# Kernel tuning notes

Measured on AMD Instinct MI355X. Metric: run time of the kernel, lower is better.

The kernel has to match this reference:

```python
import jax, jax.numpy as jnp
import numpy as np

EPS_ATTN = 1e-8  # self.eps is undefined in the torch source; standard slot-attention value
LN_EPS = 1e-5


def _ln(x, g=None, b=None, axes=(-1,)):
    m = x.mean(axes, keepdims=True)
    v = ((x - m) ** 2).mean(axes, keepdims=True)
    y = (x - m) * jax.lax.rsqrt(v + LN_EPS)
    return y * g + b if g is not None else y


def setup_inputs() -> dict:
    key = jax.random.key(0)
    ks = jax.random.split(key, 16)
    B, N, S, d, dh = 16, 4096, 8, 64, 128

    def w(k, shape, fan_in):
        return jax.random.normal(k, shape, jnp.float32) / np.float32(np.sqrt(fan_in))

    return {
        "inputs": jax.random.normal(ks[0], (B, N, d + 2), jnp.float32),
        "slots": jax.random.normal(ks[1], (S, d + 4), jnp.float32),
        "Wq": w(ks[2], (d, d), d),
        "Wk": w(ks[3], (d, d), d),
        "Wv": w(ks[4], (d, d), d),
        "Wg": w(ks[5], (d, 2), 2),
        "bg": jnp.zeros((d,), jnp.float32),
        "ln_pos_g": jnp.ones((d,), jnp.float32),
        "ln_pos_b": jnp.zeros((d,), jnp.float32),
        "W1": w(ks[6], (dh, d), d),
        "b1": jnp.zeros((dh,), jnp.float32),
        "W2": w(ks[7], (d, dh), dh),
        "b2": jnp.zeros((d,), jnp.float32),
        "W_ih": w(ks[8], (3 * d, d), d),
        "W_hh": w(ks[9], (3 * d, d), d),
        "b_ih": jnp.zeros((3 * d,), jnp.float32),
        "b_hh": jnp.zeros((3 * d,), jnp.float32),
        "ln_mlp_g": jnp.ones((d,), jnp.float32),
        "ln_mlp_b": jnp.zeros((d,), jnp.float32),
        "W3": w(ks[10], (dh, d), d),
        "b3": jnp.zeros((dh,), jnp.float32),
        "W4": w(ks[11], (d, dh), dh),
        "b4": jnp.zeros((d,), jnp.float32),
        "ln_slot_g": jnp.ones((d,), jnp.float32),
        "ln_slot_b": jnp.zeros((d,), jnp.float32),
        "n_iters": 3,
    }


def reference(inputs, slots, Wq, Wk, Wv, Wg, bg, ln_pos_g, ln_pos_b, W1, b1, W2, b2,
              W_ih, W_hh, b_ih, b_hh, ln_mlp_g, ln_mlp_b, W3, b3, W4, b4,
              ln_slot_g, ln_slot_b, n_iters):
    feats, grids = inputs[..., :-2], inputs[..., -2:]          # (B,N,d), (B,N,2)
    sl, pos, sc = slots[..., :-4], slots[..., -4:-2], slots[..., -2:]
    B, N, _ = feats.shape
    S, d = sl.shape
    scale = d ** (-0.5)

    slots = jnp.broadcast_to(sl, (B, S, d))
    positions = jnp.clip(jnp.broadcast_to(pos, (B, S, 2)), -1.0, 1.0)
    scales = jnp.clip(jnp.broadcast_to(sc, (B, S, 2)), 1e-3, 2.0)

    k = feats @ Wk.T                                           # (B,N,d)
    v = feats @ Wv.T

    def pos_mlp(x):  # LayerNorm -> Linear -> ReLU -> Linear
        h = _ln(x, ln_pos_g, ln_pos_b)
        h = jax.nn.relu(h @ W1.T + b1)
        return h @ W2.T + b2

    for i_iter in range(n_iters + 1):
        rel = (grids[:, :, None] - positions[:, None]) / scales[:, None]  # (B,N,S,2)
        rgp = rel @ Wg.T + bg                                             # (B,N,S,d)
        k_pos = pos_mlp(k[:, :, None] + rgp)                              # (B,N,S,d)
        v_pos = pos_mlp(v[:, :, None] + rgp)

        slots_n = _ln(slots, ln_slot_g, ln_slot_b)
        q = _ln(slots_n, axes=(-2, -1)) @ Wq.T                            # (B,S,d)

        dots = jnp.einsum('bsd,bnsd->bns', q, k_pos) * scale              # (B,N,S)
        attn = jax.nn.softmax(dots, axis=1) + EPS_ATTN
        attn = attn / attn.sum(axis=-1, keepdims=True)

        updates = jnp.einsum('bns,bnsd->bsd', attn, v_pos)                # (B,S,d)
        positions = jnp.einsum('bns,bnp->bsp', attn, grids)               # (B,S,2)
        spread = (grids[:, :, None] - positions[:, None]) ** 2            # (B,N,S,2)
        scales = jnp.clip(jnp.sqrt(jnp.einsum('bns,bnsp->bsp', attn, spread)), 1e-3, 2.0)

        if i_iter < n_iters:
            x = updates.reshape(-1, d)
            h = slots.reshape(-1, d)
            gi = x @ W_ih.T + b_ih
            gh = h @ W_hh.T + b_hh
            i_r, i_z, i_n = jnp.split(gi, 3, axis=-1)
            h_r, h_z, h_n = jnp.split(gh, 3, axis=-1)
            r = jax.nn.sigmoid(i_r + h_r)
            z = jax.nn.sigmoid(i_z + h_z)
            n_g = jnp.tanh(i_n + r * h_n)
            slots = ((1.0 - z) * n_g + z * h).reshape(B, S, d)
            # slot_mlp (no residual in the source)
            hmlp = jax.nn.relu(_ln(slots, ln_mlp_g, ln_mlp_b) @ W3.T + b3)
            slots = hmlp @ W4.T + b4

    return jnp.concatenate([slots, positions, scales], axis=-1)           # (B,S,d+4)
```

## Files before the change

kernel.cpp:

```cpp
#include <hip/hip_runtime.h>
#include <math.h>

#define BB 16
#define NN 4096
#define SS 8
#define DD 64
#define DHH 128
#define CIN 66
#define NITERS 3
#define LN_EPS_F 1e-5f
#define EPS_ATTN_F 1e-8f
#define QSCALE 0.125f
#define LO_SCALE 2048.0f
#define LO_INV 4.8828125e-4f

typedef __attribute__((ext_vector_type(8))) _Float16 half8;
typedef __attribute__((ext_vector_type(4))) float f32x4;
union H8 { half8 v; _Float16 u[8]; };

__device__ __forceinline__ float dot4(float4 a, float4 b) {
    return fmaf(a.x, b.x, fmaf(a.y, b.y, fmaf(a.z, b.z, a.w * b.w)));
}

__device__ __forceinline__ void split_fp16(float z, _Float16& h, _Float16& l) {
// ... 1 lines not shown
    float rem = (z - (float)hh) * LO_SCALE;
    h = hh;
    l = (_Float16)rem;
}

__global__ __launch_bounds__(256) void k_init_slots(
    const float* __restrict__ slots_in, float* __restrict__ slots,
    float* __restrict__ positions, float* __restrict__ scales) {
    int tid = blockIdx.x * 256 + threadIdx.x;
    if (tid < BB * SS * DD) {
        int s = (tid / DD) % SS;
        int c = tid % DD;
        slots[tid] = slots_in[s * 68 + c];
    }
    if (tid < BB * SS * 2) {
        int s = (tid >> 1) & 7;
        int p = tid & 1;
        float po = slots_in[s * 68 + 64 + p];
        positions[tid] = fminf(fmaxf(po, -1.f), 1.f);
        float sc = slots_in[s * 68 + 66 + p];
        scales[tid] = fminf(fmaxf(sc, 1e-3f), 2.f);
    }
}

__global__ __launch_bounds__(256) void k_prep_w(
    const float* __restrict__ W1, const float* __restrict__ lpg,
    const float* __restrict__ lpb, const float* __restrict__ b1,
    const float* __restrict__ Wg,
    float* __restrict__ W1p, float* __restrict__ avec, float* __restrict__ bvec,
    float* __restrict__ s1vec, float* __restrict__ b1p, float* __restrict__ wgc) {
    __shared__ float w1s[128 * 68];
    int tid = threadIdx.x;
    for (int q = 0; q < 8; q++) {
        int flat = q * 1024 + tid * 4;
        int o = flat >> 6, c = flat & 63;
        *(float4*)(w1s + o * 68 + c) = *(const float4*)(W1 + flat);
    }
    __syncthreads();
    if (tid < 128) {
        int o = tid;
        float a = 0.f, bv = 0.f, s1 = 0.f, b1a = b1[o];
        for (int c = 0; c < 64; c++) {
            float w0 = w1s[o * 68 + c];
            float w = w0 * lpg[c];
            W1p[o * 64 + c] = w;
            a = fmaf(w, Wg[2 * c], a);
            bv = fmaf(w, Wg[2 * c + 1], bv);
            s1 += w;
            b1a = fmaf(w0, lpb[c], b1a);
        }
        avec[o] = a; bvec[o] = bv; s1vec[o] = s1; b1p[o] = b1a;
    }
    if (tid == 128) {
        float mwA = 0.f, mwB = 0.f, AA = 0.f, BBv = 0.f, AB = 0.f;
        for (int c = 0; c < 64; c++) {
            float wa = Wg[2 * c], wb = Wg[2 * c + 1];
            mwA += wa; mwB += wb;
            AA = fmaf(wa, wa, AA); BBv = fmaf(wb, wb, BBv); AB = fmaf(wa, wb, AB);
        }
        wgc[0] = mwA * (1.f / 64.f);
        wgc[1] = mwB * (1.f / 64.f);
        wgc[2] = AA * (1.f / 64.f);
        wgc[3] = BBv * (1.f / 64.f);
        wgc[4] = AB * (2.f / 64.f);
    }
}

__global__ __launch_bounds__(256) void k_prep_w2(
    const float* __restrict__ W1p, const float* __restrict__ Wk,
    const float* __restrict__ Wv, const float* __restrict__ bg,
    float* __restrict__ Wall, float* __restrict__ cu) {
    int flat = blockIdx.x * 256 + threadIdx.x;
    int mat = flat >> 13, rem = flat & 8191;
    int o = rem >> 6, c = rem & 63;
    const float* Wm = mat ? Wv : Wk;
    float acc = 0.f;
    for (int d = 0; d < 64; d++)
        acc = fmaf(W1p[o * 64 + d], Wm[d * 64 + c], acc);
    Wall[flat] = acc;
    if (flat < 128) {
        float a = 0.f;
        for (int d = 0; d < 64; d++) a = fmaf(W1p[flat * 64 + d], bg[d], a);
        cu[flat] = a;
    }
}

__global__ __launch_bounds__(256) void k_prep_frag(
    const float* __restrict__ Wall, const float* __restrict__ Wk,
    const float* __restrict__ Wv,
    _Float16* __restrict__ cwh, _Float16* __restrict__ cwl,
    _Float16* __restrict__ mwh, _Float16* __restrict__ mwl) {
    int idx = blockIdx.x * 256 + threadIdx.x;
    if (idx < 2048) {
        int f = idx >> 6, lane = idx & 63;
        int m = f >> 4, rest = f & 15;
        int ot = rest >> 1, ks = rest & 1;
        int o = ot * 16 + (lane & 15);
        int k0 = ks * 32 + (lane >> 4) * 8;
        const float* src = Wall + m * 8192 + o * 64 + k0;
        #pragma unroll
        for (int j = 0; j < 8; j++) {
            _Float16 h, l;
            split_fp16(src[j], h, l);
            cwh[(size_t)f * 512 + lane * 8 + j] = h;
            cwl[(size_t)f * 512 + lane * 8 + j] = l;
        }
    } else if (idx < 3072) {
        int id2 = idx - 2048;
        int f = id2 >> 6, lane = id2 & 63;
        int m = f >> 3, rest = f & 7;
        int ot = rest >> 1, ks = rest & 1;
        int o = ot * 16 + (lane & 15);
        int k0 = ks * 32 + (lane >> 4) * 8;
        const float* src = (m ? Wv : Wk) + o * 64 + k0;
        #pragma unroll
        for (int j = 0; j < 8; j++) {
            _Float16 h, l;
            split_fp16(src[j], h, l);
            mwh[(size_t)f * 512 + lane * 8 + j] = h;
            mwl[(size_t)f * 512 + lane * 8 + j] = l;
        }
    }
}

__global__ __launch_bounds__(256) void k_prep_mfma(
    const float* __restrict__ inp,
    const _Float16* __restrict__ cwh, const _Float16* __restrict__ cwl,
    const _Float16* __restrict__ mwh, const _Float16* __restrict__ mwl,
    const float* __restrict__ cu, const float* __restrict__ bg,
    const float* __restrict__ Wg,
    float* __restrict__ uk, float* __restrict__ uv,
    float* __restrict__ kaux, float* __restrict__ vaux, float* __restrict__ gbuf) {
    int tid = threadIdx.x;
    int wv = tid >> 6, lane = tid & 63;
    int quad = lane >> 4, col = lane & 15;
    int mat = blockIdx.y;
    int rowTile = blockIdx.x * 64 + wv * 16;
    half8 ah[2], al[2];
    {
        int rA = rowTile + col;
        const float* rp = inp + (size_t)rA * CIN + quad * 8;
        #pragma unroll
        for (int ks = 0; ks < 2; ks++) {
            H8 h, l;
            #pragma unroll
            for (int q = 0; q < 4; q++) {
                float2 v = *(const float2*)(rp + ks * 32 + 2 * q);
                split_fp16(v.x, h.u[2 * q], l.u[2 * q]);
                split_fp16(v.y, h.u[2 * q + 1], l.u[2 * q + 1]);
            }
            ah[ks] = h.v; al[ks] = l.v;
        }
    }
    const _Float16* cwhm = cwh + (size_t)mat * 16 * 512;
    const _Float16* cwlm = cwl + (size_t)mat * 16 * 512;
    float* dst = mat ? uv : uk;
    float* outb = dst + (size_t)(rowTile + quad * 4) * 128 + col;
    #pragma unroll
    for (int ot = 0; ot < 8; ot++) {
        f32x4 acc1 = {0.f, 0.f, 0.f, 0.f}, acc2 = {0.f, 0.f, 0.f, 0.f};
        #pragma unroll
        for (int ks = 0; ks < 2; ks++) {
            half8 bh = *(const half8*)(cwhm + (size_t)(ot * 2 + ks) * 512 + lane * 8);
            half8 bl = *(const half8*)(cwlm + (size_t)(ot * 2 + ks) * 512 + lane * 8);
            acc1 = __builtin_amdgcn_mfma_f32_16x16x32_f16(ah[ks], bh, acc1, 0, 0, 0);
            acc2 = __builtin_amdgcn_mfma_f32_16x16x32_f16(al[ks], bh, acc2, 0, 0, 0);
// ... 100 lines not shown
    w2q[(b * SS + s) * DHH + c] = a0 * QSCALE;
    w2q[(b * SS + s) * DHH + c + 64] = a1 * QSCALE;
    float qb = qv[s][c] * b2[c];
    for (int off = 32; off; off >>= 1) qb += __shfl_xor(qb, off, 64);
    if (c == 0) qb2[b * SS + s] = qb * QSCALE;
}

__global__ __launch_bounds__(256) void k_pass1(
    const float* __restrict__ uk, const float* __restrict__ kaux,
    const float* __restrict__ positions, const float* __restrict__ scales,
    const float* __restrict__ avec, const float* __restrict__ bvec,
    const float* __restrict__ s1vec, const float* __restrict__ b1p,
    const float* __restrict__ wgc, const float* __restrict__ w2q,
    const float* __restrict__ qb2, float* __restrict__ dots) {
    int tid = threadIdx.x;
    int chunk = blockIdx.x, b = blockIdx.y;
    int wv = tid >> 6, lane = tid & 63, rh = lane >> 5, ol = lane & 31;
    int o4 = ol * 4;
    float4 a4 = *(const float4*)(avec + o4);
    float4 bv4 = *(const float4*)(bvec + o4);
    float4 s14 = *(const float4*)(s1vec + o4);
    float4 b14 = *(const float4*)(b1p + o4);
    float mwA = wgc[0], mwB = wgc[1], AA = wgc[2], BBc = wgc[3], AB2 = wgc[4];
    float p0[8], p1[8], rc0[8], rc1[8], qb[8];
    float4 wq[8];
    #pragma unroll
    for (int s = 0; s < 8; s++) {
        int bs = b * 8 + s;
        p0[s] = positions[bs * 2]; p1[s] = positions[bs * 2 + 1];
        rc0[s] = 1.f / scales[bs * 2]; rc1[s] = 1.f / scales[bs * 2 + 1];
        qb[s] = qb2[bs];
        wq[s] = *(const float4*)(w2q + (size_t)bs * DHH + o4);
    }
    int row0 = chunk * 64 + wv * 16 + rh;
    size_t rg = (size_t)b * NN + row0;
    float4 m1 = *(const float4*)(kaux + rg * 8);
    float4 m2 = *(const float4*)(kaux + rg * 8 + 4);
    float4 u4 = *(const float4*)(uk + rg * 128 + o4);
    for (int st = 0; st < 8; st++) {
        float4 n1, n2, nu;
        if (st < 7) {
            size_t rgn = rg + (size_t)(st + 1) * 2;
            n1 = *(const float4*)(kaux + rgn * 8);
            n2 = *(const float4*)(kaux + rgn * 8 + 4);
            nu = *(const float4*)(uk + rgn * 128 + o4);
        }
        int row = row0 + st * 2;
        #pragma unroll
        for (int s = 0; s < 8; s++) {
            float rel0 = (m2.x - p0[s]) * rc0[s];
            float rel1 = (m2.y - p1[s]) * rc1[s];
            float m = fmaf(rel1, mwB, fmaf(rel0, mwA, m1.x));
            float q2 = fmaf(rel0, fmaf(rel0, AA, m1.z), m1.y);
            q2 = fmaf(rel1, fmaf(rel1, BBc, m1.w), q2);
            q2 = fmaf(rel0 * rel1, AB2, q2);
            float var = fmaf(-m, m, q2);
            float rstd = rsqrtf(fmaxf(var, 0.f) + LN_EPS_F);
            float p = 0.f, t, h;
            t = fmaf(-m, s14.x, u4.x); t = fmaf(rel0, a4.x, t); t = fmaf(rel1, bv4.x, t);
            h = fmaf(rstd, t, b14.x); p = fmaf(fmaxf(h, 0.f), wq[s].x, p);
            t = fmaf(-m, s14.y, u4.y); t = fmaf(rel0, a4.y, t); t = fmaf(rel1, bv4.y, t);
            h = fmaf(rstd, t, b14.y); p = fmaf(fmaxf(h, 0.f), wq[s].y, p);
            t = fmaf(-m, s14.z, u4.z); t = fmaf(rel0, a4.z, t); t = fmaf(rel1, bv4.z, t);
            h = fmaf(rstd, t, b14.z); p = fmaf(fmaxf(h, 0.f), wq[s].z, p);
            t = fmaf(-m, s14.w, u4.w); t = fmaf(rel0, a4.w, t); t = fmaf(rel1, bv4.w, t);
            h = fmaf(rstd, t, b14.w); p = fmaf(fmaxf(h, 0.f), wq[s].w, p);
            p += __shfl_xor(p, 1, 64);
            p += __shfl_xor(p, 2, 64);
            p += __shfl_xor(p, 4, 64);
            p += __shfl_xor(p, 8, 64);
            p += __shfl_xor(p, 16, 64);
            if (ol == 0)
                dots[(size_t)(b * 8 + s) * NN + row] = p + qb[s];
        }
        m1 = n1; m2 = n2; u4 = nu;
    }
}

__global__ __launch_bounds__(256) void k_pass2(
    const float* __restrict__ uv, const float* __restrict__ vaux,
    const float* __restrict__ positions, const float* __restrict__ scales,
    const float* __restrict__ avec, const float* __restrict__ bvec,
    const float* __restrict__ s1vec, const float* __restrict__ b1p,
    const float* __restrict__ wgc, const float* __restrict__ attn,
    float* __restrict__ H) {
    __shared__ float Hw[4 * 1024];
    int tid = threadIdx.x;
    int chunk = blockIdx.x, b = blockIdx.y;
    int wv = tid >> 6, lane = tid & 63, rh = lane >> 5, ol = lane & 31;
    int o4 = ol * 4;
    float4 a4 = *(const float4*)(avec + o4);
    float4 bv4 = *(const float4*)(bvec + o4);
    float4 s14 = *(const float4*)(s1vec + o4);
    float4 b14 = *(const float4*)(b1p + o4);
    float mwA = wgc[0], mwB = wgc[1], AA = wgc[2], BBc = wgc[3], AB2 = wgc[4];
    float p0[8], p1[8], rc0[8], rc1[8];
    #pragma unroll
    for (int s = 0; s < 8; s++) {
        int bs = b * 8 + s;
        p0[s] = positions[bs * 2]; p1[s] = positions[bs * 2 + 1];
        rc0[s] = 1.f / scales[bs * 2]; rc1[s] = 1.f / scales[bs * 2 + 1];
    }
    float hq[8][4];
    #pragma unroll
    for (int s = 0; s < 8; s++)
        #pragma unroll
        for (int c = 0; c < 4; c++) hq[s][c] = 0.f;
    int row0 = chunk * 64 + wv * 16 + rh;
    size_t rg = (size_t)b * NN + row0;
    float4 m1 = *(const float4*)(vaux + rg * 8);
    float4 m2 = *(const float4*)(vaux + rg * 8 + 4);
    float4 u4 = *(const float4*)(uv + rg * 128 + o4);
    for (int st = 0; st < 8; st++) {
        float4 n1, n2, nu;
        if (st < 7) {
            size_t rgn = rg + (size_t)(st + 1) * 2;
            n1 = *(const float4*)(vaux + rgn * 8);
            n2 = *(const float4*)(vaux + rgn * 8 + 4);
            nu = *(const float4*)(uv + rgn * 128 + o4);
        }
        int row = row0 + st * 2;
        #pragma unroll
        for (int s = 0; s < 8; s++) {
            float ar = attn[(size_t)(b * 8 + s) * NN + row];
            float rel0 = (m2.x - p0[s]) * rc0[s];
            float rel1 = (m2.y - p1[s]) * rc1[s];
            float m = fmaf(rel1, mwB, fmaf(rel0, mwA, m1.x));
            float q2 = fmaf(rel0, fmaf(rel0, AA, m1.z), m1.y);
            q2 = fmaf(rel1, fmaf(rel1, BBc, m1.w), q2);
            q2 = fmaf(rel0 * rel1, AB2, q2);
            float var = fmaf(-m, m, q2);
            float rstd = rsqrtf(fmaxf(var, 0.f) + LN_EPS_F);
            float t, h;
            t = fmaf(-m, s14.x, u4.x); t = fmaf(rel0, a4.x, t); t = fmaf(rel1, bv4.x, t);
            h = fmaf(rstd, t, b14.x); hq[s][0] = fmaf(ar, fmaxf(h, 0.f), hq[s][0]);
            t = fmaf(-m, s14.y, u4.y); t = fmaf(rel0, a4.y, t); t = fmaf(rel1, bv4.y, t);
            h = fmaf(rstd, t, b14.y); hq[s][1] = fmaf(ar, fmaxf(h, 0.f), hq[s][1]);
            t = fmaf(-m, s14.z, u4.z); t = fmaf(rel0, a4.z, t); t = fmaf(rel1, bv4.z, t);
            h = fmaf(rstd, t, b14.z); hq[s][2] = fmaf(ar, fmaxf(h, 0.f), hq[s][2]);
            t = fmaf(-m, s14.w, u4.w); t = fmaf(rel0, a4.w, t); t = fmaf(rel1, bv4.w, t);
            h = fmaf(rstd, t, b14.w); hq[s][3] = fmaf(ar, fmaxf(h, 0.f), hq[s][3]);
        }
        m1 = n1; m2 = n2; u4 = nu;
    }
    #pragma unroll
    for (int s = 0; s < 8; s++)
        #pragma unroll
        for (int c = 0; c < 4; c++)
            hq[s][c] += __shfl_xor(hq[s][c], 32, 64);
    if (lane < 32) {
        #pragma unroll
        for (int s = 0; s < 8; s++) {
            float4 st = {hq[s][0], hq[s][1], hq[s][2], hq[s][3]};
            *(float4*)(Hw + wv * 1024 + s * 128 + o4) = st;
        }
    }
    __syncthreads();
    #pragma unroll
    for (int q = 0; q < 4; q++) {
        int flat = q * 256 + tid;
        float sum = Hw[flat] + Hw[1024 + flat] + Hw[2048 + flat] + Hw[3072 + flat];
        atomicAdd(&H[(size_t)b * 8 * DHH + flat], sum);
    }
}

__global__ __launch_bounds__(256) void k_softmax_ms(
    const float* __restrict__ dots, float* __restrict__ Mv, float* __restrict__ Lv,
    float* __restrict__ H, float* __restrict__ sacc) {
    __shared__ float red[4];
    int bs = blockIdx.x, t = threadIdx.x;
    if (t < 128) H[(size_t)bs * DHH + t] = 0.f;
    if (t < 8) sacc[bs * 8 + t] = 0.f;
    const float* dp = dots + (size_t)bs * NN;
    float mx = -1e30f;
    #pragma unroll
    for (int it = 0; it < 4; it++) {
        float4 d = *(const float4*)(dp + it * 1024 + t * 4);
        mx = fmaxf(mx, fmaxf(fmaxf(d.x, d.y), fmaxf(d.z, d.w)));
    }
    for (int off = 32; off; off >>= 1) mx = fmaxf(mx, __shfl_xor(mx, off, 64));
    if ((t & 63) == 0) red[t >> 6] = mx;
    __syncthreads();
    float M = fmaxf(fmaxf(red[0], red[1]), fmaxf(red[2], red[3]));
    __syncthreads();
    float sm = 0.f;
    #pragma unroll
    for (int it = 0; it < 4; it++) {
        float4 d = *(const float4*)(dp + it * 1024 + t * 4);
        sm += __expf(d.x - M) + __expf(d.y - M) + __expf(d.z - M) + __expf(d.w - M);
    }
    for (int off = 32; off; off >>= 1) sm += __shfl_xor(sm, off, 64);
    if ((t & 63) == 0) red[t >> 6] = sm;
    __syncthreads();
    if (t == 0) { Mv[bs] = M; Lv[bs] = red[0] + red[1] + red[2] + red[3]; }
}

__global__ __launch_bounds__(256) void k_attn_stats(
    const float* __restrict__ dots, const float* __restrict__ Mv,
    const float* __restrict__ Lv, const float* __restrict__ gbuf,
    float* __restrict__ attn, float* __restrict__ sacc) {
    __shared__ float red[4][40];
    int chunk = blockIdx.x, b = blockIdx.y;
    int t = threadIdx.x;
    int n = chunk * 256 + t;
    float2 g = *(const float2*)(gbuf + (size_t)(b * NN + n) * 2);
    float gx2 = g.x * g.x, gy2 = g.y * g.y;
    float a[8];
    float rs = 0.f;
    #pragma unroll
    for (int s = 0; s < 8; s++) {
        int bs = b * 8 + s;
        float d = dots[(size_t)bs * NN + n];
        a[s] = __expf(d - Mv[bs]) * (1.f / Lv[bs]) + EPS_ATTN_F;
        rs += a[s];
    }
    float inv = 1.f / rs;
    float v[8][5];
    #pragma unroll
    for (int s = 0; s < 8; s++) {
        float av = a[s] * inv;
        attn[(size_t)(b * 8 + s) * NN + n] = av;
        v[s][0] = av;
        v[s][1] = av * g.x;  v[s][2] = av * g.y;
        v[s][3] = av * gx2;  v[s][4] = av * gy2;
    }
    #pragma unroll
    for (int off = 1; off <= 32; off <<= 1)
        #pragma unroll
        for (int s = 0; s < 8; s++)
            #pragma unroll
            for (int j = 0; j < 5; j++)
                v[s][j] += __shfl_xor(v[s][j], off, 64);
    int lane = t & 63, wv = t >> 6;
    if (lane == 0) {
        #pragma unroll
        for (int s = 0; s < 8; s++)
            #pragma unroll
            for (int j = 0; j < 5; j++)
                red[wv][s * 5 + j] = v[s][j];
    }
    __syncthreads();
    if (t < 40) {
        float sum = red[0][t] + red[1][t] + red[2][t] + red[3][t];
        int s = t / 5, j = t % 5;
        atomicAdd(&sacc[(b * 8 + s) * 8 + j], sum);
    }
}

__global__ __launch_bounds__(64) void k_gru_mlp(
    const float* __restrict__ H, const float* __restrict__ sacc,
    const float* __restrict__ W2, const float* __restrict__ b2,
    const float* __restrict__ W_ih, const float* __restrict__ W_hh,
    const float* __restrict__ b_ih, const float* __restrict__ b_hh,
    const float* __restrict__ lmg, const float* __restrict__ lmb,
    const float* __restrict__ W3, const float* __restrict__ b3,
    const float* __restrict__ W4, const float* __restrict__ b4,
    float* __restrict__ slots, float* __restrict__ positions,
    float* __restrict__ scales) {
    int bs = blockIdx.x;
    int c = threadIdx.x;
    __shared__ float hl[DHH], ul[DD], sl[DD], yl[DD], hml[DHH];
    float A0 = sacc[bs * 8 + 0];
    if (c < 2) {
        float A1 = sacc[bs * 8 + 1 + c];
        float A2 = sacc[bs * 8 + 3 + c];
        positions[bs * 2 + c] = A1;
        float sx = A2 - A1 * A1 * (2.f - A0);
        scales[bs * 2 + c] = fminf(fmaxf(sqrtf(fmaxf(sx, 0.f)), 1e-3f), 2.f);
    }
    hl[c] = H[bs * DHH + c];
    hl[c + 64] = H[bs * DHH + 64 + c];
    float hold = slots[bs * DD + c];
    sl[c] = hold;
    __syncthreads();
    float u = A0 * b2[c];
    for (int o = 0; o < DHH; o += 4) {
        float4 w = *(const float4*)(W2 + c * DHH + o);
        u = fmaf(w.x, hl[o], fmaf(w.y, hl[o + 1], fmaf(w.z, hl[o + 2], fmaf(w.w, hl[o + 3], u))));
    }
    ul[c] = u;
    __syncthreads();
    float gir = b_ih[c], giz = b_ih[64 + c], gin = b_ih[128 + c];
    float ghr = b_hh[c], ghz = b_hh[64 + c], ghn = b_hh[128 + c];
    for (int k4 = 0; k4 < DD; k4 += 4) {
        float4 uu = *(const float4*)(ul + k4);
        float4 hh = *(const float4*)(sl + k4);
        gir += dot4(uu, *(const float4*)(W_ih + c * DD + k4));
        giz += dot4(uu, *(const float4*)(W_ih + (64 + c) * DD + k4));
        gin += dot4(uu, *(const float4*)(W_ih + (128 + c) * DD + k4));
        ghr += dot4(hh, *(const float4*)(W_hh + c * DD + k4));
        ghz += dot4(hh, *(const float4*)(W_hh + (64 + c) * DD + k4));
        ghn += dot4(hh, *(const float4*)(W_hh + (128 + c) * DD + k4));
    }
    float rg = 1.f / (1.f + expf(-(gir + ghr)));
    float zg = 1.f / (1.f + expf(-(giz + ghz)));
    float ng = tanhf(gin + rg * ghn);
    float snew = (1.f - zg) * ng + zg * hold;
    float sum = snew;
    for (int off = 32; off; off >>= 1) sum += __shfl_xor(sum, off, 64);
    float m = sum * (1.f / 64.f);
    float dv = snew - m;
    float vv = dv * dv;
    for (int off = 32; off; off >>= 1) vv += __shfl_xor(vv, off, 64);
    yl[c] = dv * rsqrtf(vv * (1.f / 64.f) + LN_EPS_F) * lmg[c] + lmb[c];
    __syncthreads();
    float h0 = b3[c], h1 = b3[64 + c];
    for (int k4 = 0; k4 < DD; k4 += 4) {
        float4 yy = *(const float4*)(yl + k4);
        h0 += dot4(yy, *(const float4*)(W3 + c * DD + k4));
        h1 += dot4(yy, *(const float4*)(W3 + (64 + c) * DD + k4));
    }
    hml[c] = fmaxf(h0, 0.f);
    hml[64 + c] = fmaxf(h1, 0.f);
    __syncthreads();
    float outv = b4[c];
    for (int o4 = 0; o4 < DHH; o4 += 4) {
        float4 hm4 = *(const float4*)(hml + o4);
        outv += dot4(hm4, *(const float4*)(W4 + c * DHH + o4));
    }
    slots[bs * DD + c] = outv;
}

__global__ __launch_bounds__(256) void k_write_out(
    const float* __restrict__ slots, const float* __restrict__ sacc,
    float* __restrict__ out) {
    int tid = blockIdx.x * 256 + threadIdx.x;
    if (tid >= BB * SS * 68) return;
    int bs = tid / 68, c = tid % 68;
    float v;
    if (c < 64) {
        v = slots[bs * 64 + c];
    } else if (c < 66) {
        v = sacc[bs * 8 + 1 + (c - 64)];
    } else {
        int p = c - 66;
        float A0 = sacc[bs * 8 + 0];
        float A1 = sacc[bs * 8 + 1 + p];
        float A2 = sacc[bs * 8 + 3 + p];
        float sx = A2 - A1 * A1 * (2.f - A0);
        v = fminf(fmaxf(sqrtf(fmaxf(sx, 0.f)), 1e-3f), 2.f);
    }
    out[tid] = v;
}

extern "C" void kernel_launch(void* const* d_in, const int* in_sizes, int n_in,
                              void* d_out, int out_size, void* d_ws, size_t ws_size,
                              hipStream_t stream) {
    (void)in_sizes; (void)n_in; (void)out_size; (void)ws_size;
    const float* inp = (const float*)d_in[0];
    const float* slots_in = (const float*)d_in[1];
    const float* Wq = (const float*)d_in[2];
    const float* Wk = (const float*)d_in[3];
    const float* Wv = (const float*)d_in[4];
    const float* Wg = (const float*)d_in[5];
    const float* bg = (const float*)d_in[6];
    const float* lpg = (const float*)d_in[7];
    const float* lpb = (const float*)d_in[8];
    const float* W1 = (const float*)d_in[9];
    const float* b1 = (const float*)d_in[10];
    const float* W2 = (const float*)d_in[11];
    const float* b2 = (const float*)d_in[12];
    const float* W_ih = (const float*)d_in[13];
    const float* W_hh = (const float*)d_in[14];
    const float* b_ih = (const float*)d_in[15];
    const float* b_hh = (const float*)d_in[16];
    const float* lmg = (const float*)d_in[17];
    const float* lmb = (const float*)d_in[18];
    const float* W3 = (const float*)d_in[19];
    const float* b3 = (const float*)d_in[20];
    const float* W4 = (const float*)d_in[21];
    const float* b4 = (const float*)d_in[22];
    const float* lsg = (const float*)d_in[23];
    const float* lsb = (const float*)d_in[24];
    float* out = (float*)d_out;
    float* ws = (float*)d_ws;

    const size_t NR = (size_t)BB * NN;
    size_t o_uk = 0;
    size_t o_uv = o_uk + NR * 128;
    size_t o_kaux = o_uv + NR * 128;
    size_t o_vaux = o_kaux + NR * 8;
    size_t o_gbuf = o_vaux + NR * 8;
    size_t o_dots = o_gbuf + NR * 2;
    size_t o_attn = o_dots + NR * SS;
    size_t o_slots = o_attn + NR * SS;
    size_t o_pos = o_slots + BB * SS * DD;
    size_t o_scl = o_pos + BB * SS * 2;
    size_t o_w2q = o_scl + BB * SS * 2;
    size_t o_qb2 = o_w2q + BB * SS * DHH;
    size_t o_Mv = o_qb2 + BB * SS;
    size_t o_Lv = o_Mv + BB * SS;
    size_t o_H = o_Lv + BB * SS;
    size_t o_sacc = o_H + BB * SS * DHH;
    size_t o_W1p = o_sacc + BB * SS * 8;
    size_t o_avec = o_W1p + DHH * DD;
    size_t o_bvec = o_avec + DHH;
    size_t o_s1v = o_bvec + DHH;
    size_t o_b1p = o_s1v + DHH;
    size_t o_wgc = o_b1p + DHH;
    size_t o_Wall = o_wgc + 8;
    size_t o_cu = o_Wall + 2 * DHH * DD;
    size_t o_cwh = o_cu + DHH;
    size_t o_cwl = o_cwh + 8192;
    size_t o_mwh = o_cwl + 8192;
    size_t o_mwl = o_mwh + 4096;

    float* uk = ws + o_uk;
    float* uv = ws + o_uv;
    float* kaux = ws + o_kaux;
    float* vaux = ws + o_vaux;
    float* gbuf = ws + o_gbuf;
    float* dots = ws + o_dots;
    float* attn = ws + o_attn;
    float* slots = ws + o_slots;
    float* positions = ws + o_pos;
    float* scales = ws + o_scl;
    float* w2q = ws + o_w2q;
    float* qb2 = ws + o_qb2;
    float* Mv = ws + o_Mv;
    float* Lv = ws + o_Lv;
    float* H = ws + o_H;
    float* sacc = ws + o_sacc;
    float* W1p = ws + o_W1p;
    float* avec = ws + o_avec;
    float* bvec = ws + o_bvec;
    float* s1v = ws + o_s1v;
    float* b1p = ws + o_b1p;
    float* wgc = ws + o_wgc;
    float* Wall = ws + o_Wall;
    float* cu = ws + o_cu;
    _Float16* cwh = (_Float16*)(ws + o_cwh);
    _Float16* cwl = (_Float16*)(ws + o_cwl);
    _Float16* mwh = (_Float16*)(ws + o_mwh);
    _Float16* mwl = (_Float16*)(ws + o_mwl);

    k_init_slots<<<32, 256, 0, stream>>>(slots_in, slots, positions, scales);
    k_prep_w<<<1, 256, 0, stream>>>(W1, lpg, lpb, b1, Wg, W1p, avec, bvec, s1v, b1p, wgc);
    k_prep_w2<<<64, 256, 0, stream>>>(W1p, Wk, Wv, bg, Wall, cu);
    k_prep_frag<<<12, 256, 0, stream>>>(Wall, Wk, Wv, cwh, cwl, mwh, mwl);
    k_prep_mfma<<<dim3(1024, 2), 256, 0, stream>>>(inp, cwh, cwl, mwh, mwl,
                                                   cu, bg, Wg, uk, uv, kaux, vaux, gbuf);

    for (int it = 0; it <= NITERS; ++it) {
        k_slot_prep<<<BB, 512, 0, stream>>>(slots, lsg, lsb, Wq, W2, b2, w2q, qb2);
        k_pass1<<<dim3(64, BB), 256, 0, stream>>>(uk, kaux, positions, scales,
                                                  avec, bvec, s1v, b1p, wgc, w2q, qb2, dots);
        k_softmax_ms<<<BB * SS, 256, 0, stream>>>(dots, Mv, Lv, H, sacc);
        k_attn_stats<<<dim3(16, BB), 256, 0, stream>>>(dots, Mv, Lv, gbuf, attn, sacc);
        if (it < NITERS) {
            k_pass2<<<dim3(64, BB), 256, 0, stream>>>(uv, vaux, positions, scales,
                                                      avec, bvec, s1v, b1p, wgc, attn, H);
            k_gru_mlp<<<BB * SS, 64, 0, stream>>>(H, sacc, W2, b2, W_ih, W_hh, b_ih, b_hh,
                                                  lmg, lmb, W3, b3, W4, b4,
                                                  slots, positions, scales);
        }
    }
    k_write_out<<<34, 256, 0, stream>>>(slots, sacc, out);
}
```

Before: 443.3 us.

## Fuse attention normalization into pass2 and slot-prep into GRU kernel

Pass2 now recomputes the normalized attention from dots and the softmax stats, and accumulates the per-slot position/spread statistics itself. This drops the separate attention-stats kernel and the attn buffer round trip in the update iterations, keeping a stats-only kernel for the final iteration. The GRU/MLP kernel is widened to one block per batch and also computes the next iteration's query projection (w2q, qb2), which removes the per-iteration slot-prep launch. The cost is redundant exp/normalize work across the 32 lanes that share a row in pass2, plus extra atomics.

```diff
diff --git a/kernel.cpp b/kernel.cpp
--- a/kernel.cpp
+++ b/kernel.cpp
@@ -373,9 +373,11 @@
     const float* __restrict__ positions, const float* __restrict__ scales,
     const float* __restrict__ avec, const float* __restrict__ bvec,
     const float* __restrict__ s1vec, const float* __restrict__ b1p,
-    const float* __restrict__ wgc, const float* __restrict__ attn,
-    float* __restrict__ H) {
+    const float* __restrict__ wgc, const float* __restrict__ dots,
+    const float* __restrict__ Mv, const float* __restrict__ Lv,
+    float* __restrict__ H, float* __restrict__ sacc) {
     __shared__ float Hw[4 * 1024];
+    __shared__ float red2[4][8][5];
     int tid = threadIdx.x;
     int chunk = blockIdx.x, b = blockIdx.y;
     int wv = tid >> 6, lane = tid & 63, rh = lane >> 5, ol = lane & 31;
@@ -385,18 +387,20 @@
     float4 s14 = *(const float4*)(s1vec + o4);
     float4 b14 = *(const float4*)(b1p + o4);
     float mwA = wgc[0], mwB = wgc[1], AA = wgc[2], BBc = wgc[3], AB2 = wgc[4];
-    float p0[8], p1[8], rc0[8], rc1[8];
+    float p0[8], p1[8], rc0[8], rc1[8], Ms[8], Li[8];
     #pragma unroll
     for (int s = 0; s < 8; s++) {
         int bs = b * 8 + s;
         p0[s] = positions[bs * 2]; p1[s] = positions[bs * 2 + 1];
         rc0[s] = 1.f / scales[bs * 2]; rc1[s] = 1.f / scales[bs * 2 + 1];
+        Ms[s] = Mv[bs]; Li[s] = 1.f / Lv[bs];
     }
     float hq[8][4];
     #pragma unroll
     for (int s = 0; s < 8; s++)
         #pragma unroll
         for (int c = 0; c < 4; c++) hq[s][c] = 0.f;
+    float sv0 = 0.f, sv1 = 0.f, sv2 = 0.f, sv3 = 0.f, sv4 = 0.f;
     int row0 = chunk * 64 + wv * 16 + rh;
     size_t rg = (size_t)b * NN + row0;
     float4 m1 = *(const float4*)(vaux + rg * 8);
@@ -411,11 +415,26 @@
             nu = *(const float4*)(uv + rgn * 128 + o4);
         }
         int row = row0 + st * 2;
+        float a[8], rs = 0.f;
         #pragma unroll
         for (int s = 0; s < 8; s++) {
-            float ar = attn[(size_t)(b * 8 + s) * NN + row];
-            float rel0 = (m2.x - p0[s]) * rc0[s];
-            float rel1 = (m2.y - p1[s]) * rc1[s];
+            float d = dots[(size_t)(b * 8 + s) * NN + row];
+            a[s] = __expf(d - Ms[s]) * Li[s] + EPS_ATTN_F;
+            rs += a[s];
+        }
+        float inv = 1.f / rs;
+        float gx = m2.x, gy = m2.y;
+        #pragma unroll
+        for (int s = 0; s < 8; s++) {
+            float ar = a[s] * inv;
+            float apv = (ol == s) ? ar : 0.f;
+            sv0 += apv;
+            sv1 = fmaf(apv, gx, sv1);
+            sv2 = fmaf(apv, gy, sv2);
+            sv3 = fmaf(apv, gx * gx, sv3);
+            sv4 = fmaf(apv, gy * gy, sv4);
+            float rel0 = (gx - p0[s]) * rc0[s];
+            float rel1 = (gy - p1[s]) * rc1[s];
             float m = fmaf(rel1, mwB, fmaf(rel0, mwA, m1.x));
             float q2 = fmaf(rel0, fmaf(rel0, AA, m1.z), m1.y);
             q2 = fmaf(rel1, fmaf(rel1, BBc, m1.w), q2);
@@ -439,12 +458,24 @@
         #pragma unroll
         for (int c = 0; c < 4; c++)
             hq[s][c] += __shfl_xor(hq[s][c], 32, 64);
+    sv0 += __shfl_xor(sv0, 32, 64);
+    sv1 += __shfl_xor(sv1, 32, 64);
+    sv2 += __shfl_xor(sv2, 32, 64);
+    sv3 += __shfl_xor(sv3, 32, 64);
+    sv4 += __shfl_xor(sv4, 32, 64);
     if (lane < 32) {
         #pragma unroll
         for (int s = 0; s < 8; s++) {
             float4 st = {hq[s][0], hq[s][1], hq[s][2], hq[s][3]};
             *(float4*)(Hw + wv * 1024 + s * 128 + o4) = st;
         }
+    }
+    if (lane < 8) {
+        red2[wv][lane][0] = sv0;
+        red2[wv][lane][1] = sv1;
+        red2[wv][lane][2] = sv2;
+        red2[wv][lane][3] = sv3;
+        red2[wv][lane][4] = sv4;
     }
     __syncthreads();
     #pragma unroll
@@ -452,6 +483,11 @@
         int flat = q * 256 + tid;
         float sum = Hw[flat] + Hw[1024 + flat] + Hw[2048 + flat] + Hw[3072 + flat];
         atomicAdd(&H[(size_t)b * 8 * DHH + flat], sum);
+    }
+    if (tid < 40) {
+        int s = tid / 5, j = tid % 5;
+        float sum = red2[0][s][j] + red2[1][s][j] + red2[2][s][j] + red2[3][s][j];
+        atomicAdd(&sacc[(b * 8 + s) * 8 + j], sum);
     }
 }
 
@@ -486,10 +522,10 @@
     if (t == 0) { Mv[bs] = M; Lv[bs] = red[0] + red[1] + red[2] + red[3]; }
 }
 
-__global__ __launch_bounds__(256) void k_attn_stats(
+__global__ __launch_bounds__(256) void k_stats_only(
     const float* __restrict__ dots, const float* __restrict__ Mv,
     const float* __restrict__ Lv, const float* __restrict__ gbuf,
-    float* __restrict__ attn, float* __restrict__ sacc) {
+    float* __restrict__ sacc) {
     __shared__ float red[4][40];
     int chunk = blockIdx.x, b = blockIdx.y;
     int t = threadIdx.x;
@@ -510,7 +546,6 @@
     #pragma unroll
     for (int s = 0; s < 8; s++) {
         float av = a[s] * inv;
-        attn[(size_t)(b * 8 + s) * NN + n] = av;
         v[s][0] = av;
         v[s][1] = av * g.x;  v[s][2] = av * g.y;
         v[s][3] = av * gx2;  v[s][4] = av * gy2;
@@ -538,7 +573,7 @@
     }
 }
 
-__global__ __launch_bounds__(64) void k_gru_mlp(
+__global__ __launch_bounds__(512) void k_gru_slot(
     const float* __restrict__ H, const float* __restrict__ sacc,
     const float* __restrict__ W2, const float* __restrict__ b2,
     const float* __restrict__ W_ih, const float* __restrict__ W_hh,
@@ -546,11 +581,18 @@
     const float* __restrict__ lmg, const float* __restrict__ lmb,
     const float* __restrict__ W3, const float* __restrict__ b3,
     const float* __restrict__ W4, const float* __restrict__ b4,
+    const float* __restrict__ lsg, const float* __restrict__ lsb,
+    const float* __restrict__ Wq,
     float* __restrict__ slots, float* __restrict__ positions,
-    float* __restrict__ scales) {
-    int bs = blockIdx.x;
-    int c = threadIdx.x;
-    __shared__ float hl[DHH], ul[DD], sl[DD], yl[DD], hml[DHH];
+    float* __restrict__ scales, float* __restrict__ w2q,
+    float* __restrict__ qb2) {
+    int b = blockIdx.x, t = threadIdx.x;
+    int s = t >> 6, c = t & 63;
+    int bs = b * 8 + s;
+    __shared__ float hl[8][DHH], ul[8][DD], sl[8][DD], yl[8][DD], hml[8][DHH];
+    __shared__ float sn[512];
+    __shared__ float qv[8][64];
+    __shared__ float wsum[8], wsum2[8];
     float A0 = sacc[bs * 8 + 0];
     if (c < 2) {
         float A1 = sacc[bs * 8 + 1 + c];
@@ -559,23 +601,23 @@
         float sx = A2 - A1 * A1 * (2.f - A0);
         scales[bs * 2 + c] = fminf(fmaxf(sqrtf(fmaxf(sx, 0.f)), 1e-3f), 2.f);
     }
-    hl[c] = H[bs * DHH + c];
-    hl[c + 64] = H[bs * DHH + 64 + c];
+    hl[s][c] = H[bs * DHH + c];
+    hl[s][c + 64] = H[bs * DHH + 64 + c];
     float hold = slots[bs * DD + c];
-    sl[c] = hold;
+    sl[s][c] = hold;
     __syncthreads();
     float u = A0 * b2[c];
     for (int o = 0; o < DHH; o += 4) {
         float4 w = *(const float4*)(W2 + c * DHH + o);
-        u = fmaf(w.x, hl[o], fmaf(w.y, hl[o + 1], fmaf(w.z, hl[o + 2], fmaf(w.w, hl[o + 3], u))));
-    }
-    ul[c] = u;
+        u = fmaf(w.x, hl[s][o], fmaf(w.y, hl[s][o + 1], fmaf(w.z, hl[s][o + 2], fmaf(w.w, hl[s][o + 3], u))));
+    }
+    ul[s][c] = u;
     __syncthreads();
     float gir = b_ih[c], giz = b_ih[64 + c], gin = b_ih[128 + c];
     float ghr = b_hh[c], ghz = b_hh[64 + c], ghn = b_hh[128 + c];
     for (int k4 = 0; k4 < DD; k4 += 4) {
-        float4 uu = *(const float4*)(ul + k4);
-        float4 hh = *(const float4*)(sl + k4);
+        float4 uu = *(const float4*)(ul[s] + k4);
+        float4 hh = *(const float4*)(sl[s] + k4);
         gir += dot4(uu, *(const float4*)(W_ih + c * DD + k4));
         giz += dot4(uu, *(const float4*)(W_ih + (64 + c) * DD + k4));
         gin += dot4(uu, *(const float4*)(W_ih + (128 + c) * DD + k4));
@@ -593,23 +635,58 @@
     float dv = snew - m;
     float vv = dv * dv;
     for (int off = 32; off; off >>= 1) vv += __shfl_xor(vv, off, 64);
-    yl[c] = dv * rsqrtf(vv * (1.f / 64.f) + LN_EPS_F) * lmg[c] + lmb[c];
+    yl[s][c] = dv * rsqrtf(vv * (1.f / 64.f) + LN_EPS_F) * lmg[c] + lmb[c];
     __syncthreads();
     float h0 = b3[c], h1 = b3[64 + c];
     for (int k4 = 0; k4 < DD; k4 += 4) {
-        float4 yy = *(const float4*)(yl + k4);
+        float4 yy = *(const float4*)(yl[s] + k4);
         h0 += dot4(yy, *(const float4*)(W3 + c * DD + k4));
         h1 += dot4(yy, *(const float4*)(W3 + (64 + c) * DD + k4));
     }
-    hml[c] = fmaxf(h0, 0.f);
-    hml[64 + c] = fmaxf(h1, 0.f);
+    hml[s][c] = fmaxf(h0, 0.f);
+    hml[s][64 + c] = fmaxf(h1, 0.f);
     __syncthreads();
     float outv = b4[c];
     for (int o4 = 0; o4 < DHH; o4 += 4) {
-        float4 hm4 = *(const float4*)(hml + o4);
+        float4 hm4 = *(const float4*)(hml[s] + o4);
         outv += dot4(hm4, *(const float4*)(W4 + c * DHH + o4));
     }
     slots[bs * DD + c] = outv;
+    float x = outv;
+    float sum2 = x;
+    for (int off = 32; off; off >>= 1) sum2 += __shfl_xor(sum2, off, 64);
+    float mm = sum2 * (1.f / 64.f);
+    float dv2 = x - mm;
+    float vs = dv2 * dv2;
+    for (int off = 32; off; off >>= 1) vs += __shfl_xor(vs, off, 64);
+    float y = dv2 * rsqrtf(vs * (1.f / 64.f) + LN_EPS_F) * lsg[c] + lsb[c];
+    float s1 = y, s2 = y * y;
+    for (int off = 32; off; off >>= 1) { s1 += __shfl_xor(s1, off, 64); s2 += __shfl_xor(s2, off, 64); }
+    if (c == 0) { wsum[s] = s1; wsum2[s] = s2; }
+    __syncthreads();
+    float ts1 = 0.f, ts2 = 0.f;
+    #pragma unroll
+    for (int i = 0; i < 8; i++) { ts1 += wsum[i]; ts2 += wsum2[i]; }
+    float gm = ts1 * (1.f / 512.f);
+    float gv = ts2 * (1.f / 512.f) - gm * gm;
+    sn[t] = (y - gm) * rsqrtf(gv + LN_EPS_F);
+    __syncthreads();
+    float acc = 0.f;
+    for (int j4 = 0; j4 < 64; j4 += 4)
+        acc += dot4(*(const float4*)&sn[s * 64 + j4], *(const float4*)(Wq + c * 64 + j4));
+    qv[s][c] = acc;
+    __syncthreads();
+    float a0 = 0.f, a1 = 0.f;
+    for (int cc = 0; cc < 64; cc++) {
+        float qc = qv[s][cc];
+        a0 = fmaf(qc, W2[cc * DHH + c], a0);
+        a1 = fmaf(qc, W2[cc * DHH + c + 64], a1);
+    }
+    w2q[bs * DHH + c] = a0 * QSCALE;
+    w2q[bs * DHH + c + 64] = a1 * QSCALE;
+    float qb = qv[s][c] * b2[c];
+    for (int off = 32; off; off >>= 1) qb += __shfl_xor(qb, off, 64);
+    if (c == 0) qb2[bs] = qb * QSCALE;
 }
 
 __global__ __launch_bounds__(256) void k_write_out(
@@ -673,8 +750,7 @@
     size_t o_vaux = o_kaux + NR * 8;
     size_t o_gbuf = o_vaux + NR * 8;
     size_t o_dots = o_gbuf + NR * 2;
-    size_t o_attn = o_dots + NR * SS;
-    size_t o_slots = o_attn + NR * SS;
+    size_t o_slots = o_dots + NR * SS;
     size_t o_pos = o_slots + BB * SS * DD;
     size_t o_scl = o_pos + BB * SS * 2;
     size_t o_w2q = o_scl + BB * SS * 2;
@@ -702,7 +778,6 @@
     float* vaux = ws + o_vaux;
     float* gbuf = ws + o_gbuf;
     float* dots = ws + o_dots;
-    float* attn = ws + o_attn;
     float* slots = ws + o_slots;
     float* positions = ws + o_pos;
     float* scales = ws + o_scl;
@@ -731,19 +806,21 @@
     k_prep_frag<<<12, 256, 0, stream>>>(Wall, Wk, Wv, cwh, cwl, mwh, mwl);
     k_prep_mfma<<<dim3(1024, 2), 256, 0, stream>>>(inp, cwh, cwl, mwh, mwl,
                                                    cu, bg, Wg, uk, uv, kaux, vaux, gbuf);
+    k_slot_prep<<<BB, 512, 0, stream>>>(slots, lsg, lsb, Wq, W2, b2, w2q, qb2);
 
     for (int it = 0; it <= NITERS; ++it) {
-        k_slot_prep<<<BB, 512, 0, stream>>>(slots, lsg, lsb, Wq, W2, b2, w2q, qb2);
         k_pass1<<<dim3(64, BB), 256, 0, stream>>>(uk, kaux, positions, scales,
                                                   avec, bvec, s1v, b1p, wgc, w2q, qb2, dots);
         k_softmax_ms<<<BB * SS, 256, 0, stream>>>(dots, Mv, Lv, H, sacc);
-        k_attn_stats<<<dim3(16, BB), 256, 0, stream>>>(dots, Mv, Lv, gbuf, attn, sacc);
         if (it < NITERS) {
             k_pass2<<<dim3(64, BB), 256, 0, stream>>>(uv, vaux, positions, scales,
-                                                      avec, bvec, s1v, b1p, wgc, attn, H);
-            k_gru_mlp<<<BB * SS, 64, 0, stream>>>(H, sacc, W2, b2, W_ih, W_hh, b_ih, b_hh,
-                                                  lmg, lmb, W3, b3, W4, b4,
-                                                  slots, positions, scales);
+                                                      avec, bvec, s1v, b1p, wgc,
+                                                      dots, Mv, Lv, H, sacc);
+            k_gru_slot<<<BB, 512, 0, stream>>>(H, sacc, W2, b2, W_ih, W_hh, b_ih, b_hh,
+                                               lmg, lmb, W3, b3, W4, b4, lsg, lsb, Wq,
+                                               slots, positions, scales, w2q, qb2);
+        } else {
+            k_stats_only<<<dim3(16, BB), 256, 0, stream>>>(dots, Mv, Lv, gbuf, sacc);
         }
     }
     k_write_out<<<34, 256, 0, stream>>>(slots, sacc, out);
```

Result: slower. 553.6 us (+24.9%).

## Fuse attention normalization and stats into pass2; pre-transpose GRU/MLP weights

Applied to the files above, without the earlier changes.

Removes the separate attention-stats kernel and the attn buffer on the first three iterations. pass2 now recomputes the normalized attention from dots, Mv and Lv and accumulates the positional stats into sacc with atomics. A stats-only kernel remains for the final iteration. Separately, the GRU/MLP weights are transposed once at setup so k_gru_mlp reads them coalesced across threads. The cost is extra exp work repeated for each lane in pass2.

```diff
diff --git a/kernel.cpp b/kernel.cpp
--- a/kernel.cpp
+++ b/kernel.cpp
@@ -107,6 +107,36 @@
         float a = 0.f;
         for (int d = 0; d < 64; d++) a = fmaf(W1p[flat * 64 + d], bg[d], a);
         cu[flat] = a;
+    }
+}
+
+__global__ __launch_bounds__(256) void k_prep_wT(
+    const float* __restrict__ W2, const float* __restrict__ W_ih,
+    const float* __restrict__ W_hh, const float* __restrict__ W3,
+    const float* __restrict__ W4,
+    float* __restrict__ W2T, float* __restrict__ W_ihT,
+    float* __restrict__ W_hhT, float* __restrict__ W3T,
+    float* __restrict__ W4T) {
+    int i = blockIdx.x * 256 + threadIdx.x;
+    if (i < 8192) {
+        int o = i >> 6, c = i & 63;
+        W2T[o * 64 + c] = W2[c * 128 + o];
+    } else if (i < 20480) {
+        int j = i - 8192;
+        int k = j / 192, g = j % 192;
+        W_ihT[k * 192 + g] = W_ih[g * 64 + k];
+    } else if (i < 32768) {
+        int j = i - 20480;
+        int k = j / 192, g = j % 192;
+        W_hhT[k * 192 + g] = W_hh[g * 64 + k];
+    } else if (i < 40960) {
+        int j = i - 32768;
+        int k = j >> 7, o = j & 127;
+        W3T[k * 128 + o] = W3[o * 64 + k];
+    } else {
+        int j = i - 40960;
+        int o = j >> 6, c = j & 63;
+        W4T[o * 64 + c] = W4[c * 128 + o];
     }
 }
 
@@ -373,9 +403,11 @@
     const float* __restrict__ positions, const float* __restrict__ scales,
     const float* __restrict__ avec, const float* __restrict__ bvec,
     const float* __restrict__ s1vec, const float* __restrict__ b1p,
-    const float* __restrict__ wgc, const float* __restrict__ attn,
-    float* __restrict__ H) {
+    const float* __restrict__ wgc, const float* __restrict__ dots,
+    const float* __restrict__ Mv, const float* __restrict__ Lv,
+    float* __restrict__ H, float* __restrict__ sacc) {
     __shared__ float Hw[4 * 1024];
+    __shared__ float red2[4][8][5];
     int tid = threadIdx.x;
     int chunk = blockIdx.x, b = blockIdx.y;
     int wv = tid >> 6, lane = tid & 63, rh = lane >> 5, ol = lane & 31;
@@ -385,18 +417,20 @@
     float4 s14 = *(const float4*)(s1vec + o4);
     float4 b14 = *(const float4*)(b1p + o4);
     float mwA = wgc[0], mwB = wgc[1], AA = wgc[2], BBc = wgc[3], AB2 = wgc[4];
-    float p0[8], p1[8], rc0[8], rc1[8];
+    float p0[8], p1[8], rc0[8], rc1[8], Ms[8], Li[8];
     #pragma unroll
     for (int s = 0; s < 8; s++) {
         int bs = b * 8 + s;
         p0[s] = positions[bs * 2]; p1[s] = positions[bs * 2 + 1];
         rc0[s] = 1.f / scales[bs * 2]; rc1[s] = 1.f / scales[bs * 2 + 1];
+        Ms[s] = Mv[bs]; Li[s] = 1.f / Lv[bs];
     }
     float hq[8][4];
     #pragma unroll
     for (int s = 0; s < 8; s++)
         #pragma unroll
         for (int c = 0; c < 4; c++) hq[s][c] = 0.f;
+    float sv0 = 0.f, sv1 = 0.f, sv2 = 0.f, sv3 = 0.f, sv4 = 0.f;
     int row0 = chunk * 64 + wv * 16 + rh;
     size_t rg = (size_t)b * NN + row0;
     float4 m1 = *(const float4*)(vaux + rg * 8);
@@ -411,11 +445,26 @@
             nu = *(const float4*)(uv + rgn * 128 + o4);
         }
         int row = row0 + st * 2;
+        float a[8], rs = 0.f;
         #pragma unroll
         for (int s = 0; s < 8; s++) {
-            float ar = attn[(size_t)(b * 8 + s) * NN + row];
-            float rel0 = (m2.x - p0[s]) * rc0[s];
-            float rel1 = (m2.y - p1[s]) * rc1[s];
+            float d = dots[(size_t)(b * 8 + s) * NN + row];
+            a[s] = __expf(d - Ms[s]) * Li[s] + EPS_ATTN_F;
+            rs += a[s];
+        }
+        float inv = 1.f / rs;
+        float gx = m2.x, gy = m2.y;
+        #pragma unroll
+        for (int s = 0; s < 8; s++) {
+            float ar = a[s] * inv;
+            float apv = (ol == s) ? ar : 0.f;
+            sv0 += apv;
+            sv1 = fmaf(apv, gx, sv1);
+            sv2 = fmaf(apv, gy, sv2);
+            sv3 = fmaf(apv, gx * gx, sv3);
+            sv4 = fmaf(apv, gy * gy, sv4);
+            float rel0 = (gx - p0[s]) * rc0[s];
+            float rel1 = (gy - p1[s]) * rc1[s];
             float m = fmaf(rel1, mwB, fmaf(rel0, mwA, m1.x));
             float q2 = fmaf(rel0, fmaf(rel0, AA, m1.z), m1.y);
             q2 = fmaf(rel1, fmaf(rel1, BBc, m1.w), q2);
@@ -439,12 +488,24 @@
         #pragma unroll
         for (int c = 0; c < 4; c++)
             hq[s][c] += __shfl_xor(hq[s][c], 32, 64);
+    sv0 += __shfl_xor(sv0, 32, 64);
+    sv1 += __shfl_xor(sv1, 32, 64);
+    sv2 += __shfl_xor(sv2, 32, 64);
+    sv3 += __shfl_xor(sv3, 32, 64);
+    sv4 += __shfl_xor(sv4, 32, 64);
     if (lane < 32) {
         #pragma unroll
         for (int s = 0; s < 8; s++) {
             float4 st = {hq[s][0], hq[s][1], hq[s][2], hq[s][3]};
             *(float4*)(Hw + wv * 1024 + s * 128 + o4) = st;
         }
+    }
+    if (lane < 8) {
+        red2[wv][lane][0] = sv0;
+        red2[wv][lane][1] = sv1;
+        red2[wv][lane][2] = sv2;
+        red2[wv][lane][3] = sv3;
+        red2[wv][lane][4] = sv4;
     }
     __syncthreads();
     #pragma unroll
@@ -452,6 +513,11 @@
         int flat = q * 256 + tid;
         float sum = Hw[flat] + Hw[1024 + flat] + Hw[2048 + flat] + Hw[3072 + flat];
         atomicAdd(&H[(size_t)b * 8 * DHH + flat], sum);
+    }
+    if (tid < 40) {
+        int s = tid / 5, j = tid % 5;
+        float sum = red2[0][s][j] + red2[1][s][j] + red2[2][s][j] + red2[3][s][j];
+        atomicAdd(&sacc[(b * 8 + s) * 8 + j], sum);
     }
 }
 
@@ -486,10 +552,10 @@
     if (t == 0) { Mv[bs] = M; Lv[bs] = red[0] + red[1] + red[2] + red[3]; }
 }
 
-__global__ __launch_bounds__(256) void k_attn_stats(
+__global__ __launch_bounds__(256) void k_stats_only(
     const float* __restrict__ dots, const float* __restrict__ Mv,
     const float* __restrict__ Lv, const float* __restrict__ gbuf,
-    float* __restrict__ attn, float* __restrict__ sacc) {
+    float* __restrict__ sacc) {
     __shared__ float red[4][40];
     int chunk = blockIdx.x, b = blockIdx.y;
     int t = threadIdx.x;
@@ -510,7 +576,6 @@
     #pragma unroll
     for (int s = 0; s < 8; s++) {
         float av = a[s] * inv;
-        attn[(size_t)(b * 8 + s) * NN + n] = av;
         v[s][0] = av;
         v[s][1] = av * g.x;  v[s][2] = av * g.y;
         v[s][3] = av * gx2;  v[s][4] = av * gy2;
@@ -540,12 +605,12 @@
 
 __global__ __launch_bounds__(64) void k_gru_mlp(
     const float* __restrict__ H, const float* __restrict__ sacc,
-    const float* __restrict__ W2, const float* __restrict__ b2,
-    const float* __restrict__ W_ih, const float* __restrict__ W_hh,
+    const float* __restrict__ W2T, const float* __restrict__ b2,
+    const float* __restrict__ W_ihT, const float* __restrict__ W_hhT,
     const float* __restrict__ b_ih, const float* __restrict__ b_hh,
     const float* __restrict__ lmg, const float* __restrict__ lmb,
-    const float* __restrict__ W3, const float* __restrict__ b3,
-    const float* __restrict__ W4, const float* __restrict__ b4,
+    const float* __restrict__ W3T, const float* __restrict__ b3,
+    const float* __restrict__ W4T, const float* __restrict__ b4,
     float* __restrict__ slots, float* __restrict__ positions,
     float* __restrict__ scales) {
     int bs = blockIdx.x;
@@ -565,26 +630,27 @@
     sl[c] = hold;
     __syncthreads();
     float u = A0 * b2[c];
-    for (int o = 0; o < DHH; o += 4) {
-        float4 w = *(const float4*)(W2 + c * DHH + o);
-        u = fmaf(w.x, hl[o], fmaf(w.y, hl[o + 1], fmaf(w.z, hl[o + 2], fmaf(w.w, hl[o + 3], u))));
-    }
+    #pragma unroll 8
+    for (int o = 0; o < DHH; o++)
+        u = fmaf(W2T[o * 64 + c], hl[o], u);
     ul[c] = u;
     __syncthreads();
     float gir = b_ih[c], giz = b_ih[64 + c], gin = b_ih[128 + c];
     float ghr = b_hh[c], ghz = b_hh[64 + c], ghn = b_hh[128 + c];
-    for (int k4 = 0; k4 < DD; k4 += 4) {
-        float4 uu = *(const float4*)(ul + k4);
-        float4 hh = *(const float4*)(sl + k4);
-        gir += dot4(uu, *(const float4*)(W_ih + c * DD + k4));
-        giz += dot4(uu, *(const float4*)(W_ih + (64 + c) * DD + k4));
-        gin += dot4(uu, *(const float4*)(W_ih + (128 + c) * DD + k4));
-        ghr += dot4(hh, *(const float4*)(W_hh + c * DD + k4));
-        ghz += dot4(hh, *(const float4*)(W_hh + (64 + c) * DD + k4));
-        ghn += dot4(hh, *(const float4*)(W_hh + (128 + c) * DD + k4));
-    }
-    float rg = 1.f / (1.f + expf(-(gir + ghr)));
-    float zg = 1.f / (1.f + expf(-(giz + ghz)));
+    #pragma unroll 4
+    for (int k = 0; k < DD; k++) {
+        float uu = ul[k], hh = sl[k];
+        const float* wi = W_ihT + k * 192 + c;
+        const float* wh = W_hhT + k * 192 + c;
+        gir = fmaf(uu, wi[0], gir);
+        giz = fmaf(uu, wi[64], giz);
+        gin = fmaf(uu, wi[128], gin);
+        ghr = fmaf(hh, wh[0], ghr);
+        ghz = fmaf(hh, wh[64], ghz);
+        ghn = fmaf(hh, wh[128], ghn);
+    }
+    float rg = 1.f / (1.f + __expf(-(gir + ghr)));
+    float zg = 1.f / (1.f + __expf(-(giz + ghz)));
     float ng = tanhf(gin + rg * ghn);
     float snew = (1.f - zg) * ng + zg * hold;
     float sum = snew;
@@ -596,19 +662,20 @@
     yl[c] = dv * rsqrtf(vv * (1.f / 64.f) + LN_EPS_F) * lmg[c] + lmb[c];
     __syncthreads();
     float h0 = b3[c], h1 = b3[64 + c];
-    for (int k4 = 0; k4 < DD; k4 += 4) {
-        float4 yy = *(const float4*)(yl + k4);
-        h0 += dot4(yy, *(const float4*)(W3 + c * DD + k4));
-        h1 += dot4(yy, *(const float4*)(W3 + (64 + c) * DD + k4));
+    #pragma unroll 4
+    for (int k = 0; k < DD; k++) {
+        float yy = yl[k];
+        const float* w3 = W3T + k * 128 + c;
+        h0 = fmaf(yy, w3[0], h0);
+        h1 = fmaf(yy, w3[64], h1);
     }
     hml[c] = fmaxf(h0, 0.f);
     hml[64 + c] = fmaxf(h1, 0.f);
     __syncthreads();
     float outv = b4[c];
-    for (int o4 = 0; o4 < DHH; o4 += 4) {
-        float4 hm4 = *(const float4*)(hml + o4);
-        outv += dot4(hm4, *(const float4*)(W4 + c * DHH + o4));
-    }
+    #pragma unroll 8
+    for (int o = 0; o < DHH; o++)
+        outv = fmaf(hml[o], W4T[o * 64 + c], outv);
     slots[bs * DD + c] = outv;
 }
 
@@ -673,8 +740,7 @@
     size_t o_vaux = o_kaux + NR * 8;
     size_t o_gbuf = o_vaux + NR * 8;
     size_t o_dots = o_gbuf + NR * 2;
-    size_t o_attn = o_dots + NR * SS;
-    size_t o_slots = o_attn + NR * SS;
+    size_t o_slots = o_dots + NR * SS;
     size_t o_pos = o_slots + BB * SS * DD;
     size_t o_scl = o_pos + BB * SS * 2;
     size_t o_w2q = o_scl + BB * SS * 2;
@@ -695,6 +761,11 @@
     size_t o_cwl = o_cwh + 8192;
     size_t o_mwh = o_cwl + 8192;
     size_t o_mwl = o_mwh + 4096;
+    size_t o_W2T = o_mwl + 4096;
+    size_t o_ihT = o_W2T + 8192;
+    size_t o_hhT = o_ihT + 12288;
+    size_t o_W3T = o_hhT + 12288;
+    size_t o_W4T = o_W3T + 8192;
 
     float* uk = ws + o_uk;
     float* uv = ws + o_uv;
@@ -702,7 +773,6 @@
     float* vaux = ws + o_vaux;
     float* gbuf = ws + o_gbuf;
     float* dots = ws + o_dots;
-    float* attn = ws + o_attn;
     float* slots = ws + o_slots;
     float* positions = ws + o_pos;
     float* scales = ws + o_scl;
@@ -724,8 +794,15 @@
     _Float16* cwl = (_Float16*)(ws + o_cwl);
     _Float16* mwh = (_Float16*)(ws + o_mwh);
     _Float16* mwl = (_Float16*)(ws + o_mwl);
+    float* W2T = ws + o_W2T;
+    float* W_ihT = ws + o_ihT;
+    float* W_hhT = ws + o_hhT;
+    float* W3T = ws + o_W3T;
+    float* W4T = ws + o_W4T;
 
     k_init_slots<<<32, 256, 0, stream>>>(slots_in, slots, positions, scales);
+    k_prep_wT<<<192, 256, 0, stream>>>(W2, W_ih, W_hh, W3, W4,
+                                       W2T, W_ihT, W_hhT, W3T, W4T);
     k_prep_w<<<1, 256, 0, stream>>>(W1, lpg, lpb, b1, Wg, W1p, avec, bvec, s1v, b1p, wgc);
     k_prep_w2<<<64, 256, 0, stream>>>(W1p, Wk, Wv, bg, Wall, cu);
     k_prep_frag<<<12, 256, 0, stream>>>(Wall, Wk, Wv, cwh, cwl, mwh, mwl);
@@ -737,13 +814,15 @@
         k_pass1<<<dim3(64, BB), 256, 0, stream>>>(uk, kaux, positions, scales,
                                                   avec, bvec, s1v, b1p, wgc, w2q, qb2, dots);
         k_softmax_ms<<<BB * SS, 256, 0, stream>>>(dots, Mv, Lv, H, sacc);
-        k_attn_stats<<<dim3(16, BB), 256, 0, stream>>>(dots, Mv, Lv, gbuf, attn, sacc);
         if (it < NITERS) {
             k_pass2<<<dim3(64, BB), 256, 0, stream>>>(uv, vaux, positions, scales,
-                                                      avec, bvec, s1v, b1p, wgc, attn, H);
-            k_gru_mlp<<<BB * SS, 64, 0, stream>>>(H, sacc, W2, b2, W_ih, W_hh, b_ih, b_hh,
-                                                  lmg, lmb, W3, b3, W4, b4,
-                                                  slots, positions, scales);
+                                                      avec, bvec, s1v, b1p, wgc,
+                                                      dots, Mv, Lv, H, sacc);
+            k_gru_mlp<<<BB * SS, 64, 0, stream>>>(H, sacc, W2T, b2, W_ihT, W_hhT,
+                                                  b_ih, b_hh, lmg, lmb, W3T, b3,
+                                                  W4T, b4, slots, positions, scales);
+        } else {
+            k_stats_only<<<dim3(16, BB), 256, 0, stream>>>(dots, Mv, Lv, gbuf, sacc);
         }
     }
     k_write_out<<<34, 256, 0, stream>>>(slots, sacc, out);
```

New measurement: 486.2 us. +9.7%, slower.
